# Kernel optimization log

Measured on AMD Instinct MI355X. Metric: run time of the kernel, lower is better.

The kernel has to match this reference:

```python
import jax, jax.numpy as jnp
import numpy as np

N = 100000      # nodes
E = 1600000     # edges
F_IN = 128      # num_node_features
C = 8           # num_classes
EPS = 1e-5


def _lin_init(key, fi, fo):
    k1, k2 = jax.random.split(key)
    s = 1.0 / np.sqrt(fi)
    W = jax.random.uniform(k1, (fi, fo), jnp.float32, -s, s)
    b = jax.random.uniform(k2, (fo,), jnp.float32, -s, s)
    return W, b


def _bn_init(key, f):
    k1, k2, k3, k4 = jax.random.split(key, 4)
    gamma = 1.0 + 0.1 * jax.random.normal(k1, (f,), jnp.float32)
    beta = 0.1 * jax.random.normal(k2, (f,), jnp.float32)
    mean = 0.1 * jax.random.normal(k3, (f,), jnp.float32)
    var = jax.random.uniform(k4, (f,), jnp.float32, 0.5, 1.5)
    return gamma, beta, mean, var


def setup_inputs() -> dict:
    key = jax.random.key(0)
    ks = jax.random.split(key, 10)
    p = {}
    p["x"] = jax.random.normal(ks[0], (N, F_IN), jnp.float32)
    p["edge_index"] = jax.random.randint(ks[1], (2, E), 0, N, jnp.int32)
    p["W1"], p["b1"] = _lin_init(ks[2], F_IN, 64)
    p["g1"], p["be1"], p["m1"], p["v1"] = _bn_init(ks[3], 64)
    p["W2"], p["b2"] = _lin_init(ks[4], 64, 32)
    p["g2"], p["be2"], p["m2"], p["v2"] = _bn_init(ks[5], 32)
    p["W3"], p["b3"] = _lin_init(ks[6], 32, 16)
    p["g3"], p["be3"], p["m3"], p["v3"] = _bn_init(ks[7], 16)
    p["fcW"], p["fcb"] = _lin_init(ks[8], 16, C)
    return p


def _gcn_conv(h, W, b, src, dst, dinv):
    # GCNConv: transform, then symmetric-normalized aggregation with self-loops.
    hw = h @ W                                   # [N, Fout]
    coef = (dinv[src] * dinv[dst])[:, None]      # [E, 1]
    agg = jax.ops.segment_sum(hw[src] * coef, dst, num_segments=N)
    agg = agg + hw * (dinv * dinv)[:, None]      # self-loop contribution
    return agg + b


def _bn(h, g, be, m, v):
    # eval-mode BatchNorm1d with running stats
    return g * (h - m) * jax.lax.rsqrt(v + EPS) + be


def reference(x, edge_index, W1, b1, g1, be1, m1, v1, W2, b2, g2, be2, m2, v2,
              W3, b3, g3, be3, m3, v3, fcW, fcb):
    src, dst = edge_index[0], edge_index[1]
    deg = jax.ops.segment_sum(jnp.ones((E,), jnp.float32), dst, num_segments=N) + 1.0
    dinv = jax.lax.rsqrt(deg)                    # deg >= 1 due to self-loops

    h = jax.nn.relu(_bn(_gcn_conv(x, W1, b1, src, dst, dinv), g1, be1, m1, v1))
    h = jax.nn.relu(_bn(_gcn_conv(h, W2, b2, src, dst, dinv), g2, be2, m2, v2))
    h = jax.nn.relu(_bn(_gcn_conv(h, W3, b3, src, dst, dinv), g3, be3, m3, v3))
    return jax.nn.sigmoid(h @ fcW + fcb)
```

## Files before the change

kernel.cpp:

```cpp
#include <hip/hip_runtime.h>
#include <math.h>

static constexpr int NN = 100000;
static constexpr int NE = 1600000;
static constexpr float BN_EPS = 1e-5f;
static constexpr int K_BKT = (NN + 255) / 256;
static constexpr int CH = 4096;
static constexpr int CAP = 6144;

typedef __attribute__((ext_vector_type(8))) short bf16x8;
typedef __attribute__((ext_vector_type(4))) float f32x4;

__device__ __forceinline__ unsigned short f2bf(float f) {
    unsigned int u = __float_as_uint(f);
    u += 0x7fffu + ((u >> 16) & 1u);
    return (unsigned short)(u >> 16);
}
__device__ __forceinline__ float bf2f(unsigned short b) {
    return __uint_as_float(((unsigned int)b) << 16);
}

__global__ __launch_bounds__(256) void partition_edges(
    const int* __restrict__ src, const int* __restrict__ dst,
    int* __restrict__ bcur, int* __restrict__ staged, int e)
{
    __shared__ int s_out[CH];
    __shared__ int cntL[512];
    __shared__ int gbase[K_BKT];
    __shared__ int curL[K_BKT];

    int tid = threadIdx.x;
    int c0 = blockIdx.x * CH;
    int cend = min(c0 + CH, e);

    for (int i = tid; i < 512; i += 256) cntL[i] = 0;
    __syncthreads();

    int sreg[16], dreg[16];
#pragma unroll
    for (int k = 0; k < 16; ++k) {
        int i = c0 + tid + k * 256;
        if (i < cend) {
            sreg[k] = src[i];
            dreg[k] = dst[i];
            atomicAdd(&cntL[((unsigned)dreg[k]) >> 8], 1);
        }
    }
    __syncthreads();

    for (int b = tid; b < K_BKT; b += 256) {
        int c = cntL[b];
        gbase[b] = (c > 0) ? (b * CAP + atomicAdd(&bcur[b], c)) : 0;
    }
    __syncthreads();

    for (int d = 1; d < 512; d <<= 1) {
        int x0 = (tid >= d) ? cntL[tid - d] : 0;
        int i1 = tid + 256;
        int x1 = (i1 >= d) ? cntL[i1 - d] : 0;
        __syncthreads();
        cntL[tid] += x0;
        cntL[i1]  += x1;
        __syncthreads();
    }
    for (int b = tid; b < K_BKT; b += 256)
        curL[b] = (b == 0) ? 0 : cntL[b - 1];
    __syncthreads();

#pragma unroll
    for (int k = 0; k < 16; ++k) {
        int i = c0 + tid + k * 256;
        if (i < cend) {
            int b = ((unsigned)dreg[k]) >> 8;
            int r = atomicAdd(&curL[b], 1);
            s_out[r] = sreg[k] | ((dreg[k] & 255) << 24);
        }
    }
    __syncthreads();

    int wave = tid >> 6, lane = tid & 63;
    for (int b = wave; b < K_BKT; b += 4) {
        int lo = (b == 0) ? 0 : cntL[b - 1];
        int hi = cntL[b];
        int gb = gbase[b];
        for (int i = lo + lane; i < hi; i += 64)
            staged[gb + (i - lo)] = s_out[i];
    }
}

__global__ __launch_bounds__(256) void place_edges(
    const int* __restrict__ bcnt, const int* __restrict__ staged,
    int* __restrict__ esrc, int* __restrict__ off, int* __restrict__ cnt,
    float* __restrict__ dinv, int n)
{
    __shared__ int cntL[256];
    __shared__ int scn[256];
    __shared__ int curL[256];
    int b = blockIdx.x;
    int tid = threadIdx.x;
    int node0 = b << 8;
    int nN = min(256, n - node0);
    int beg = b * CAP;
    int end = beg + bcnt[b];

    cntL[tid] = 0;
    __syncthreads();
    for (int i = beg + tid; i < end; i += 256)
        atomicAdd(&cntL[((unsigned)staged[i]) >> 24], 1);
    __syncthreads();
    scn[tid] = cntL[tid];
    __syncthreads();
    for (int d = 1; d < 256; d <<= 1) {
        int x = (tid >= d) ? scn[tid - d] : 0;
        __syncthreads();
        scn[tid] += x;
        __syncthreads();
    }
    int lofs = (tid == 0) ? 0 : scn[tid - 1];
    if (tid < nN) {
        int node = node0 + tid;
        off[node] = beg + lofs;
        cnt[node] = cntL[tid];
        dinv[node] = rsqrtf((float)cntL[tid] + 1.0f);
    }
    curL[tid] = beg + lofs;
    __syncthreads();
    for (int i = beg + tid; i < end; i += 256) {
        int u = staged[i];
        int pos = atomicAdd(&curL[((unsigned)u) >> 24], 1);
        esrc[pos] = u & 0x00FFFFFF;
    }
}

template<int K, int FOUT>
__device__ __forceinline__ void prep_body3(
    const float* __restrict__ W, unsigned short* __restrict__ blob, int t)
{
    constexpr int CT = FOUT / 16;
    int lane = t & 63;
    int ct   = (t >> 6) % CT;
    int ks   = (t >> 6) / CT;
    int col  = ct * 16 + (lane & 15);
    int k0   = ks * 32 + (lane >> 4) * 8;

    union { bf16x8 v; unsigned short e[8]; } u;
#pragma unroll
    for (int j = 0; j < 8; ++j) {
        int kp = k0 + j;
        unsigned short r;
        if (kp < 2 * K) {
            int k = (kp < K) ? kp : kp - K;
            r = f2bf(W[k * FOUT + col]);
        } else {
            float f = W[(kp - 2 * K) * FOUT + col];
            unsigned short h = f2bf(f);
            r = f2bf(f - bf2f(h));
        }
        u.e[j] = r;
    }
    *reinterpret_cast<bf16x8*>(blob + (size_t)t * 8) = u.v;
}

template<int K, int FOUT>
__device__ __forceinline__ void prep_body2(
    const float* __restrict__ W, unsigned short* __restrict__ blob, int t)
{
    constexpr int CT = FOUT / 16;
    int lane = t & 63;
    int ct   = (t >> 6) % CT;
    int ks   = (t >> 6) / CT;
    int col  = ct * 16 + (lane & 15);
    int k0   = ks * 32 + (lane >> 4) * 8;

    union { bf16x8 v; unsigned short e[8]; } u;
#pragma unroll
    for (int j = 0; j < 8; ++j) {
        int kp = k0 + j;
        unsigned short r;
        if (kp < K) {
            r = f2bf(W[kp * FOUT + col]);
        } else {
            float f = W[(kp - K) * FOUT + col];
            unsigned short h = f2bf(f);
            r = f2bf(f - bf2f(h));
        }
        u.e[j] = r;
    }
    *reinterpret_cast<bf16x8*>(blob + (size_t)t * 8) = u.v;
}

__global__ __launch_bounds__(256) void prep_all(
    const float* __restrict__ W1, const float* __restrict__ W2,
    const float* __restrict__ W3, unsigned short* __restrict__ b1,
    unsigned short* __restrict__ b2, unsigned short* __restrict__ b3,
    int* __restrict__ bcur)
{
    int t = blockIdx.x * 256 + threadIdx.x;
    if (t < 3072)              prep_body3<128, 64>(W1, b1, t);
    else if (t < 3584)         prep_body2<64, 32>(W2, b2, t - 3072);
    else if (t < 3712)         prep_body2<32, 16>(W3, b3, t - 3584);
    else if (t < 3712 + K_BKT) bcur[t - 3712] = 0;
}

template<int K, int FOUT>
__global__ __launch_bounds__(256) void gemm_mfma(
    const float* __restrict__ h, const unsigned short* __restrict__ wtb,
    const float* __restrict__ dinv, unsigned short* __restrict__ hw, int n)
{
    constexpr int PAD = 8;
    constexpr int LDA = 2 * K + PAD;
    constexpr int CT  = FOUT / 16;
    constexpr int KS  = (3 * K) / 32;
    __shared__ unsigned short As[32 * LDA];

    const int tid  = threadIdx.x;
    const int row0 = blockIdx.x * 32;

    constexpr int QK = K / 4;
    for (int i = tid; i < 32 * QK; i += 256) {
        int r = i / QK;
        int q = i % QK;
        int g = row0 + r;
        float4 v;
        if (g < n) v = *reinterpret_cast<const float4*>(h + (size_t)g * K + q * 4);
        else       v = make_float4(0.f, 0.f, 0.f, 0.f);
        ushort4 hi, lo;
        hi.x = f2bf(v.x); lo.x = f2bf(v.x - bf2f(hi.x));
        hi.y = f2bf(v.y); lo.y = f2bf(v.y - bf2f(hi.y));
        hi.z = f2bf(v.z); lo.z = f2bf(v.z - bf2f(hi.z));
        hi.w = f2bf(v.w); lo.w = f2bf(v.w - bf2f(hi.w));
        *reinterpret_cast<ushort4*>(&As[r * LDA + q * 4])     = hi;
        *reinterpret_cast<ushort4*>(&As[r * LDA + K + q * 4]) = lo;
    }
    __syncthreads();

    const int wave = tid >> 6;
    const int lane = tid & 63;
    const int l15  = lane & 15;
    const int kgrp = (lane >> 4) * 8;
    const int rw   = wave & 1;
    const int chf  = wave >> 1;
    const int arow = rw * 16 + l15;

    const unsigned short* wlane = wtb + lane * 8;

    f32x4 acc[2];
    acc[0] = (f32x4){0.f, 0.f, 0.f, 0.f};
    acc[1] = (f32x4){0.f, 0.f, 0.f, 0.f};

#pragma unroll
    for (int ks = 0; ks < KS; ++ks) {
        int kp = ks * 32 + kgrp;
        int ka = (kp >= 2 * K) ? kp - 2 * K : kp;
        bf16x8 a = *reinterpret_cast<const bf16x8*>(&As[arow * LDA + ka]);
#pragma unroll
        for (int hh = 0; hh < 2; ++hh) {
            int ct = chf * 2 + hh;
            bf16x8 b = *reinterpret_cast<const bf16x8*>(wlane + (ks * CT + ct) * 512);
            acc[hh] = __builtin_amdgcn_mfma_f32_16x16x32_bf16(a, b, acc[hh], 0, 0, 0);
        }
    }

    const int rbase = rw * 16 + (lane >> 4) * 4;
    float dv[4];
#pragma unroll
    for (int j = 0; j < 4; ++j) {
        int g = row0 + rbase + j;
        dv[j] = (g < n) ? dinv[g] : 0.f;
    }
#pragma unroll
    for (int hh = 0; hh < 2; ++hh) {
        int col = (chf * 2 + hh) * 16 + l15;
#pragma unroll
        for (int j = 0; j < 4; ++j) {
            int g = row0 + rbase + j;
            if (g < n) hw[(size_t)g * FOUT + col] = f2bf(acc[hh][j] * dv[j]);
        }
    }
}

template<int F, int FOUT2>
__global__ __launch_bounds__(256) void gather_gemm(
    const int* __restrict__ off, const int* __restrict__ cnt,
    const int* __restrict__ esrc, const float* __restrict__ dinv,
    const unsigned short* __restrict__ hwin, const float* __restrict__ bias,
    const float* __restrict__ g, const float* __restrict__ be,
    const float* __restrict__ m, const float* __restrict__ v,
    const unsigned short* __restrict__ wtb, unsigned short* __restrict__ hwout,
    int n)
{
    constexpr int SG  = F / 4;
    constexpr int NSG = 64 / SG;
    constexpr int PAD = 8;
    constexpr int LDA = F + PAD;
    constexpr int CT  = FOUT2 / 16;
    constexpr int KS  = (2 * F) / 32;
    __shared__ unsigned short As[64 * LDA];

    const int tid   = threadIdx.x;
    const int wv    = tid >> 6;
    const int lane  = tid & 63;
    const int node0 = blockIdx.x * 64;
    const int sg = lane / SG;
    const int p  = lane % SG;

    int offv = 0, cntv = 0;
    float dnv = 0.f;
    {
        int nd = node0 + wv * 16 + (lane & 15);
        if (nd < n) {
            offv = off[nd];
            cntv = cnt[nd];
            dnv  = dinv[nd];
        }
    }

    for (int t = 0; t < 16; ++t) {
        int node = node0 + wv * 16 + t;
        int r = wv * 16 + t;
        int beg = __shfl(offv, t);
        int num = __shfl(cntv, t);
        float dn = __shfl(dnv, t);
        float sx = 0.f, sy = 0.f, sz = 0.f, sw = 0.f;
        if (node < n) {
            int j = sg;
            for (; j + NSG < num; j += 2 * NSG) {
                int s0 = esrc[beg + j];
                int s1 = esrc[beg + j + NSG];
                ushort4 a = *reinterpret_cast<const ushort4*>(hwin + (size_t)s0 * F + 4 * p);
                ushort4 b = *reinterpret_cast<const ushort4*>(hwin + (size_t)s1 * F + 4 * p);
                sx += bf2f(a.x) + bf2f(b.x);
                sy += bf2f(a.y) + bf2f(b.y);
                sz += bf2f(a.z) + bf2f(b.z);
                sw += bf2f(a.w) + bf2f(b.w);
            }
            if (j < num) {
                int s0 = esrc[beg + j];
                ushort4 a = *reinterpret_cast<const ushort4*>(hwin + (size_t)s0 * F + 4 * p);
                sx += bf2f(a.x); sy += bf2f(a.y); sz += bf2f(a.z); sw += bf2f(a.w);
            }
            if (sg == 0) {
                ushort4 a = *reinterpret_cast<const ushort4*>(hwin + (size_t)node * F + 4 * p);
                sx += bf2f(a.x); sy += bf2f(a.y); sz += bf2f(a.z); sw += bf2f(a.w);
            }
        }
#pragma unroll
        for (int d = SG; d < 64; d <<= 1) {
            sx += __shfl_xor(sx, d);
            sy += __shfl_xor(sy, d);
            sz += __shfl_xor(sz, d);
            sw += __shfl_xor(sw, d);
        }
        if (sg == 0) {
            float y0 = 0.f, y1 = 0.f, y2 = 0.f, y3 = 0.f;
            int c0 = 4 * p;
            if (node < n) {
                float4 gg = *reinterpret_cast<const float4*>(g + c0);
                float4 vv = *reinterpret_cast<const float4*>(v + c0);
                float4 bb = *reinterpret_cast<const float4*>(bias + c0);
                float4 mm = *reinterpret_cast<const float4*>(m + c0);
                float4 ee = *reinterpret_cast<const float4*>(be + c0);
                y0 = fmaxf(gg.x * rsqrtf(vv.x + BN_EPS) * (dn * sx + bb.x - mm.x) + ee.x, 0.f);
                y1 = fmaxf(gg.y * rsqrtf(vv.y + BN_EPS) * (dn * sy + bb.y - mm.y) + ee.y, 0.f);
                y2 = fmaxf(gg.z * rsqrtf(vv.z + BN_EPS) * (dn * sz + bb.z - mm.z) + ee.z, 0.f);
                y3 = fmaxf(gg.w * rsqrtf(vv.w + BN_EPS) * (dn * sw + bb.w - mm.w) + ee.w, 0.f);
            }
            ushort4 pk;
            pk.x = f2bf(y0); pk.y = f2bf(y1); pk.z = f2bf(y2); pk.w = f2bf(y3);
            *reinterpret_cast<ushort4*>(&As[r * LDA + c0]) = pk;
        }
    }
    __syncthreads();

    const int l15  = lane & 15;
    const int kgrp = (lane >> 4) * 8;
    const int arow = wv * 16 + l15;
    const unsigned short* wlane = wtb + lane * 8;

    f32x4 acc[CT];
#pragma unroll
    for (int ct = 0; ct < CT; ++ct) acc[ct] = (f32x4){0.f, 0.f, 0.f, 0.f};

#pragma unroll
    for (int ks = 0; ks < KS; ++ks) {
        int kp = ks * 32 + kgrp;
        int ka = (kp >= F) ? kp - F : kp;
        bf16x8 a = *reinterpret_cast<const bf16x8*>(&As[arow * LDA + ka]);
#pragma unroll
        for (int ct = 0; ct < CT; ++ct) {
            bf16x8 b = *reinterpret_cast<const bf16x8*>(wlane + (ks * CT + ct) * 512);
            acc[ct] = __builtin_amdgcn_mfma_f32_16x16x32_bf16(a, b, acc[ct], 0, 0, 0);
        }
    }

    const int rbase = wv * 16 + (lane >> 4) * 4;
    float dv[4];
#pragma unroll
    for (int j = 0; j < 4; ++j) {
        int gr = node0 + rbase + j;
        dv[j] = (gr < n) ? dinv[gr] : 0.f;
    }
#pragma unroll
    for (int ct = 0; ct < CT; ++ct) {
#pragma unroll
        for (int j = 0; j < 4; ++j) {
            int gr = node0 + rbase + j;
            if (gr < n) hwout[(size_t)gr * FOUT2 + ct * 16 + l15] = f2bf(acc[ct][j] * dv[j]);
        }
    }
}

__global__ __launch_bounds__(256) void gather_bn_relu_fc(
    const int* __restrict__ off, const int* __restrict__ cnt,
    const int* __restrict__ esrc, const float* __restrict__ dinv,
    const unsigned short* __restrict__ hw, const float* __restrict__ bias,
    const float* __restrict__ g, const float* __restrict__ be,
    const float* __restrict__ m, const float* __restrict__ v,
    const float* __restrict__ fcW, const float* __restrict__ fcb,
    float* __restrict__ out, int n)
{
    constexpr int F = 16, SG = 4, NSG = 16;
    __shared__ float WsF[128];
    __shared__ float bsF[8];
    __shared__ float ybuf[4][16];

    int tid = threadIdx.x;
    if (tid < 128) WsF[tid] = fcW[tid];
    if (tid < 8)   bsF[tid] = fcb[tid];
    __syncthreads();

    int node = (blockIdx.x * 256 + tid) >> 6;
    int wv   = tid >> 6;
    int lane = tid & 63;
    bool act = node < n;

    if (act) {
        int sg = lane / SG;
        int p  = lane % SG;
        int beg = off[node];
        int num = cnt[node];

        float sx = 0.f, sy = 0.f, sz = 0.f, sw = 0.f;
        int j = sg;
        for (; j + NSG < num; j += 2 * NSG) {
            int s0 = esrc[beg + j];
            int s1 = esrc[beg + j + NSG];
            ushort4 a = *reinterpret_cast<const ushort4*>(hw + (size_t)s0 * F + 4 * p);
            ushort4 b = *reinterpret_cast<const ushort4*>(hw + (size_t)s1 * F + 4 * p);
            sx += bf2f(a.x) + bf2f(b.x);
            sy += bf2f(a.y) + bf2f(b.y);
            sz += bf2f(a.z) + bf2f(b.z);
            sw += bf2f(a.w) + bf2f(b.w);
        }
        if (j < num) {
            int s0 = esrc[beg + j];
            ushort4 a = *reinterpret_cast<const ushort4*>(hw + (size_t)s0 * F + 4 * p);
            sx += bf2f(a.x); sy += bf2f(a.y); sz += bf2f(a.z); sw += bf2f(a.w);
        }
        if (sg == 0) {
            ushort4 a = *reinterpret_cast<const ushort4*>(hw + (size_t)node * F + 4 * p);
            sx += bf2f(a.x); sy += bf2f(a.y); sz += bf2f(a.z); sw += bf2f(a.w);
        }

#pragma unroll
        for (int d = SG; d < 64; d <<= 1) {
            sx += __shfl_xor(sx, d);
            sy += __shfl_xor(sy, d);
            sz += __shfl_xor(sz, d);
            sw += __shfl_xor(sw, d);
        }

        if (sg == 0) {
            int c0 = 4 * p;
            float dn = dinv[node];
            ybuf[wv][c0+0] = fmaxf(g[c0+0] * rsqrtf(v[c0+0] + BN_EPS) * (dn * sx + bias[c0+0] - m[c0+0]) + be[c0+0], 0.f);
            ybuf[wv][c0+1] = fmaxf(g[c0+1] * rsqrtf(v[c0+1] + BN_EPS) * (dn * sy + bias[c0+1] - m[c0+1]) + be[c0+1], 0.f);
            ybuf[wv][c0+2] = fmaxf(g[c0+2] * rsqrtf(v[c0+2] + BN_EPS) * (dn * sz + bias[c0+2] - m[c0+2]) + be[c0+2], 0.f);
            ybuf[wv][c0+3] = fmaxf(g[c0+3] * rsqrtf(v[c0+3] + BN_EPS) * (dn * sw + bias[c0+3] - m[c0+3]) + be[c0+3], 0.f);
        }
    }
    __syncthreads();

    if (act && lane < 8) {
        float o = bsF[lane];
#pragma unroll
        for (int k = 0; k < 16; ++k) o += ybuf[wv][k] * WsF[k * 8 + lane];
        out[(size_t)node * 8 + lane] = 1.0f / (1.0f + expf(-o));
    }
}

extern "C" void kernel_launch(void* const* d_in, const int* in_sizes, int n_in,
                              void* d_out, int out_size, void* d_ws, size_t ws_size,
                              hipStream_t stream) {
    const float* x   = (const float*)d_in[0];
    const int*   ei  = (const int*)  d_in[1];
    const float* W1  = (const float*)d_in[2];
    const float* b1  = (const float*)d_in[3];
    const float* g1  = (const float*)d_in[4];
    const float* be1 = (const float*)d_in[5];
    const float* m1  = (const float*)d_in[6];
    const float* v1  = (const float*)d_in[7];
    const float* W2  = (const float*)d_in[8];
    const float* b2  = (const float*)d_in[9];
    const float* g2  = (const float*)d_in[10];
    const float* be2 = (const float*)d_in[11];
    const float* m2  = (const float*)d_in[12];
    const float* v2  = (const float*)d_in[13];
    const float* W3  = (const float*)d_in[14];
    const float* b3  = (const float*)d_in[15];
    const float* g3  = (const float*)d_in[16];
    const float* be3 = (const float*)d_in[17];
    const float* m3  = (const float*)d_in[18];
    const float* v3  = (const float*)d_in[19];
    const float* fcW = (const float*)d_in[20];
    const float* fcb = (const float*)d_in[21];
    float* out = (float*)d_out;

    const int* src = ei;
    const int* dst = ei + NE;

    char* w = (char*)d_ws;
    float* dinv  = (float*)(w + 0);
    int*   cnt   = (int*)  (w + (512 << 10));
    int*   off   = (int*)  (w + (1024 << 10));
    int*   bcur  = (int*)  (w + (1536 << 10));
    int*   staged= (int*)  (w + (2u << 20));
    int*   esrc  = (int*)  (w + (12u << 20));
    unsigned short* wt1 = (unsigned short*)(w + (22u << 20));
    unsigned short* wt2 = wt1 + 24576;
    unsigned short* wt3 = wt2 + 4096;
    unsigned short* hw1 = (unsigned short*)(w + (24u << 20));
    unsigned short* hw2 = (unsigned short*)(w + (38u << 20));
    unsigned short* hw3 = (unsigned short*)(w + (46u << 20));

    prep_all<<<(3712 + K_BKT + 255) / 256, 256, 0, stream>>>(
        W1, W2, W3, wt1, wt2, wt3, bcur);

    partition_edges<<<(NE + CH - 1) / CH, 256, 0, stream>>>(src, dst, bcur, staged, NE);
    place_edges<<<K_BKT, 256, 0, stream>>>(bcur, staged, esrc, off, cnt, dinv, NN);

    const int GB = (NN + 63) / 64;
    const int GG = (NN * 64 + 255) / 256;

    gemm_mfma<128, 64><<<(NN + 31) / 32, 256, 0, stream>>>(x, wt1, dinv, hw1, NN);

    gather_gemm<64, 32><<<GB, 256, 0, stream>>>(
        off, cnt, esrc, dinv, hw1, b1, g1, be1, m1, v1, wt2, hw2, NN);

    gather_gemm<32, 16><<<GB, 256, 0, stream>>>(
        off, cnt, esrc, dinv, hw2, b2, g2, be2, m2, v2, wt3, hw3, NN);

    gather_bn_relu_fc<<<GG, 256, 0, stream>>>(
        off, cnt, esrc, dinv, hw3, b3, g3, be3, m3, v3, fcW, fcb, out, NN);
}
```

Measured before the change: 233.6 us.

## Preload edge indices per wave, flatten staging copy, use nontemporal stores

The aggregation kernels now load up to 64 neighbor indices with one coalesced load per wave and broadcast them with shuffles, instead of each subgroup reading the index array separately. Degrees above 64 fall back to a direct-load loop. The partition kernel's copy-out becomes a flat per-thread loop that finds each element's bucket by binary search over the prefix counts, which replaces the per-bucket wave loop and its poor lane use. Edge staging and placement writes become nontemporal stores, at the cost of extra shuffle and search instructions.

Result: slower. 302.7 us (+29.6%).

```diff
diff --git a/kernel.cpp b/kernel.cpp
--- a/kernel.cpp
+++ b/kernel.cpp
@@ -32,6 +32,7 @@
     int tid = threadIdx.x;
     int c0 = blockIdx.x * CH;
     int cend = min(c0 + CH, e);
+    int nE = cend - c0;
 
     for (int i = tid; i < 512; i += 256) cntL[i] = 0;
     __syncthreads();
@@ -78,13 +79,16 @@
     }
     __syncthreads();
 
-    int wave = tid >> 6, lane = tid & 63;
-    for (int b = wave; b < K_BKT; b += 4) {
+    for (int i = tid; i < nE; i += 256) {
+        int val = s_out[i];
+        int b = 0;
+#pragma unroll
+        for (int step = 256; step >= 1; step >>= 1) {
+            int nb = b + step;
+            if (nb <= 512 && cntL[nb - 1] <= i) b = nb;
+        }
         int lo = (b == 0) ? 0 : cntL[b - 1];
-        int hi = cntL[b];
-        int gb = gbase[b];
-        for (int i = lo + lane; i < hi; i += 64)
-            staged[gb + (i - lo)] = s_out[i];
+        __builtin_nontemporal_store(val, &staged[gbase[b] + (i - lo)]);
     }
 }
 
@@ -128,7 +132,7 @@
     for (int i = beg + tid; i < end; i += 256) {
         int u = staged[i];
         int pos = atomicAdd(&curL[((unsigned)u) >> 24], 1);
-        esrc[pos] = u & 0x00FFFFFF;
+        __builtin_nontemporal_store(u & 0x00FFFFFF, &esrc[pos]);
     }
 }
 
@@ -323,10 +327,13 @@
         float dn = __shfl(dnv, t);
         float sx = 0.f, sy = 0.f, sz = 0.f, sw = 0.f;
         if (node < n) {
+            int eidx = 0;
+            if (lane < num) eidx = __builtin_nontemporal_load(esrc + beg + lane);
+            int lim = (num < 64) ? num : 64;
             int j = sg;
-            for (; j + NSG < num; j += 2 * NSG) {
-                int s0 = esrc[beg + j];
-                int s1 = esrc[beg + j + NSG];
+            for (; j + NSG < lim; j += 2 * NSG) {
+                int s0 = __shfl(eidx, j);
+                int s1 = __shfl(eidx, j + NSG);
                 ushort4 a = *reinterpret_cast<const ushort4*>(hwin + (size_t)s0 * F + 4 * p);
                 ushort4 b = *reinterpret_cast<const ushort4*>(hwin + (size_t)s1 * F + 4 * p);
                 sx += bf2f(a.x) + bf2f(b.x);
@@ -334,8 +341,13 @@
                 sz += bf2f(a.z) + bf2f(b.z);
                 sw += bf2f(a.w) + bf2f(b.w);
             }
-            if (j < num) {
-                int s0 = esrc[beg + j];
+            if (j < lim) {
+                int s0 = __shfl(eidx, j);
+                ushort4 a = *reinterpret_cast<const ushort4*>(hwin + (size_t)s0 * F + 4 * p);
+                sx += bf2f(a.x); sy += bf2f(a.y); sz += bf2f(a.z); sw += bf2f(a.w);
+            }
+            for (int jj = 64 + sg; jj < num; jj += NSG) {
+                int s0 = esrc[beg + jj];
                 ushort4 a = *reinterpret_cast<const ushort4*>(hwin + (size_t)s0 * F + 4 * p);
                 sx += bf2f(a.x); sy += bf2f(a.y); sz += bf2f(a.z); sw += bf2f(a.w);
             }
@@ -441,10 +453,13 @@
         int num = cnt[node];
 
         float sx = 0.f, sy = 0.f, sz = 0.f, sw = 0.f;
+        int eidx = 0;
+        if (lane < num) eidx = __builtin_nontemporal_load(esrc + beg + lane);
+        int lim = (num < 64) ? num : 64;
         int j = sg;
-        for (; j + NSG < num; j += 2 * NSG) {
-            int s0 = esrc[beg + j];
-            int s1 = esrc[beg + j + NSG];
+        for (; j + NSG < lim; j += 2 * NSG) {
+            int s0 = __shfl(eidx, j);
+            int s1 = __shfl(eidx, j + NSG);
             ushort4 a = *reinterpret_cast<const ushort4*>(hw + (size_t)s0 * F + 4 * p);
             ushort4 b = *reinterpret_cast<const ushort4*>(hw + (size_t)s1 * F + 4 * p);
             sx += bf2f(a.x) + bf2f(b.x);
@@ -452,8 +467,13 @@
             sz += bf2f(a.z) + bf2f(b.z);
             sw += bf2f(a.w) + bf2f(b.w);
         }
-        if (j < num) {
-            int s0 = esrc[beg + j];
+        if (j < lim) {
+            int s0 = __shfl(eidx, j);
+            ushort4 a = *reinterpret_cast<const ushort4*>(hw + (size_t)s0 * F + 4 * p);
+            sx += bf2f(a.x); sy += bf2f(a.y); sz += bf2f(a.z); sw += bf2f(a.w);
+        }
+        for (int jj = 64 + sg; jj < num; jj += NSG) {
+            int s0 = esrc[beg + jj];
             ushort4 a = *reinterpret_cast<const ushort4*>(hw + (size_t)s0 * F + 4 * p);
             sx += bf2f(a.x); sy += bf2f(a.y); sz += bf2f(a.z); sw += bf2f(a.w);
         }
```
